# Optimization experiments

Hardware: AMD Instinct MI355X
Metric: run time of the kernel (lower is better)

Reference implementation:

```python
import jax, jax.numpy as jnp
import numpy as np
from jax import lax

BS = 256
EPS = 1e-5  # torch LayerNorm default


def _layernorm(x, g, b):
    m = jnp.mean(x, axis=-1, keepdims=True)
    v = jnp.var(x, axis=-1, keepdims=True)
    return (x - m) / jnp.sqrt(v + EPS) * g + b


def _conv(x, w, b):
    y = lax.conv_general_dilated(x, w, (1, 1), 'VALID',
                                 dimension_numbers=('NCHW', 'OIHW', 'NCHW'))
    return y + b[None, :, None, None]


def _maxpool2(x):
    return lax.reduce_window(x, -jnp.inf, lax.max, (1, 1, 2, 2), (1, 1, 2, 2), 'VALID')


def setup_inputs() -> dict:
    key = jax.random.key(0)
    ks = iter(jax.random.split(key, 64))
    def rn(shape, scale=0.05):
        return jax.random.normal(next(ks), shape, dtype=jnp.float32) * scale
    return dict(
        t=jax.random.uniform(next(ks), (BS, 128, 128), dtype=jnp.float32) * 255.0,
        conv1_w=rn((32, 1, 3, 3)), conv1_b=rn((32,)),
        conv2_w=rn((32, 32, 3, 3)), conv2_b=rn((32,)),
        exp_w=rn((36, 64)), exp_b=rn((64,)),
        # 16 tile-attention modules x 4 heads x (64 -> 16)
        mh_wq=rn((16, 4, 64, 16)), mh_bq=rn((16, 4, 16)),
        mh_wk=rn((16, 4, 64, 16)), mh_bk=rn((16, 4, 16)),
        mh_wv=rn((16, 4, 64, 16)), mh_bv=rn((16, 4, 16)),
        mh_wo=rn((16, 64, 64)), mh_bo=rn((16, 64)),
        ln1_g=jnp.ones((64,), jnp.float32), ln1_b=jnp.zeros((64,), jnp.float32),
        # 2 XL layers x 8 heads x (2048 -> 256)
        xl_wq=rn((2, 8, 2048, 256)), xl_bq=rn((2, 8, 256)),
        xl_wk=rn((2, 8, 2048, 256)), xl_bk=rn((2, 8, 256)),
        xl_wv=rn((2, 8, 2048, 256)), xl_bv=rn((2, 8, 256)),
        xl_wo=rn((2, 2048, 2048)), xl_bo=rn((2, 2048)),
        xln_g=jnp.ones((2, 2048), jnp.float32), xln_b=jnp.zeros((2, 2048), jnp.float32),
        fl1_w=rn((32768, 512)), fl1_b=rn((512,)),
        fl2_w=rn((512, 128)), fl2_b=rn((128,)),
        fl3_w=rn((128, 25)), fl3_b=rn((25,)),
    )


def reference(t, conv1_w, conv1_b, conv2_w, conv2_b, exp_w, exp_b,
              mh_wq, mh_bq, mh_wk, mh_bk, mh_wv, mh_bv, mh_wo, mh_bo,
              ln1_g, ln1_b,
              xl_wq, xl_bq, xl_wk, xl_bk, xl_wv, xl_bv, xl_wo, xl_bo,
              xln_g, xln_b, fl1_w, fl1_b, fl2_w, fl2_b, fl3_w, fl3_b):
    # Eval-mode forward with discard_mem=True (fresh KV memory): every
    # AttentionHead attends over the current step only; dropout = identity.
    bs = t.shape[0]
    x = t / 255.0
    # 4x4 tiling of 32x32 patches -> (bs*16, 1, 32, 32)
    sliced = x.reshape(bs, 4, 32, 4, 32).transpose(0, 1, 3, 2, 4)
    x = sliced.reshape(bs * 16, 1, 32, 32)
    u = _maxpool2(_conv(x, conv1_w, conv1_b))        # (bs*16, 32, 15, 15)
    u = _maxpool2(_conv(u, conv2_w, conv2_b))        # (bs*16, 32, 6, 6)
    u = u.reshape(bs * 16, 32, 36)
    u = jax.nn.relu(u @ exp_w + exp_b)               # (bs*16, 32, 64)
    u = u.reshape(16, bs, 32, 64)                    # raw reshape, as in source

    # 16 multihead modules, 4 heads each, d_feature=16, seq_len=32
    q = jnp.einsum('mbsd,mhdf->mbhsf', u, mh_wq) + mh_bq[:, None, :, None, :]
    k = jnp.einsum('mbsd,mhdf->mbhsf', u, mh_wk) + mh_bk[:, None, :, None, :]
    v = jnp.einsum('mbsd,mhdf->mbhsf', u, mh_wv) + mh_bv[:, None, :, None, :]
    a = jax.nn.softmax(jnp.einsum('mbhsf,mbhtf->mbhst', q, k) / jnp.sqrt(16.0), axis=-1)
    o = jnp.einsum('mbhst,mbhtf->mbhsf', a, v)
    o = o.transpose(0, 1, 3, 2, 4).reshape(16, bs, 32, 64)  # concat heads
    o = jnp.einsum('mbsd,mde->mbse', o, mh_wo) + mh_bo[:, None, None, :]
    u = _layernorm(u + o, ln1_g, ln1_b)
    u = u.reshape(16, bs, 2048).transpose(1, 0, 2)   # (bs, 16, 2048)

    # XL stage (as written in source: att output is computed but discarded,
    # u = u + dropout(u) -> 2u under identity dropout, then LayerNorm)
    for i in range(2):
        q = jnp.einsum('bsd,hdf->bhsf', u, xl_wq[i]) + xl_bq[i][None, :, None, :]
        k = jnp.einsum('bsd,hdf->bhsf', u, xl_wk[i]) + xl_bk[i][None, :, None, :]
        vv = jnp.einsum('bsd,hdf->bhsf', u, xl_wv[i]) + xl_bv[i][None, :, None, :]
        aw = jax.nn.softmax(jnp.einsum('bhsf,bhtf->bhst', q, k) / jnp.sqrt(256.0), axis=-1)
        oo = jnp.einsum('bhst,bhtf->bhsf', aw, vv).transpose(0, 2, 1, 3).reshape(bs, 16, 2048)
        oo = oo @ xl_wo[i] + xl_bo[i]  # discarded, matching the source
        u = u + u
        u = _layernorm(u, xln_g[i], xln_b[i])

    u = u.reshape(bs, 16 * 2048)
    u = jax.nn.relu(u @ fl1_w + fl1_b)
    u = jax.nn.relu(u @ fl2_w + fl2_b)
    return u @ fl3_w + fl3_b
```

## Files before the change

### kernel.cpp

```cpp
#include <hip/hip_runtime.h>
#include <hip/hip_bf16.h>
#include <math.h>

#define LN_EPS 1e-5f

typedef __attribute__((ext_vector_type(8))) short short8v;
typedef __attribute__((ext_vector_type(4))) float f32x4;

static __device__ __forceinline__ unsigned short f2bf(float x) {
    unsigned u = __float_as_uint(x);
    u += 0x7fffu + ((u >> 16) & 1u);
    return (unsigned short)(u >> 16);
}
static __device__ __forceinline__ float bf2f(unsigned short h) {
    return __uint_as_float(((unsigned)h) << 16);
}

#define MFMA3(ACC, AH, AL, BH, BL)                                          \
    ACC = __builtin_amdgcn_mfma_f32_16x16x32_bf16(AH, BH, ACC, 0, 0, 0);    \
    ACC = __builtin_amdgcn_mfma_f32_16x16x32_bf16(AL, BH, ACC, 0, 0, 0);    \
    ACC = __builtin_amdgcn_mfma_f32_16x16x32_bf16(AH, BL, ACC, 0, 0, 0);

__global__ __launch_bounds__(512, 4) void k_fused(
    const float* __restrict__ t,
    const float* __restrict__ c1w, const float* __restrict__ c1b,
    const float* __restrict__ c2w, const float* __restrict__ c2b,
    const float* __restrict__ ew,  const float* __restrict__ eb,
    const float* __restrict__ wq, const float* __restrict__ bq,
    const float* __restrict__ wk, const float* __restrict__ bk,
    const float* __restrict__ wv, const float* __restrict__ bv,
    const float* __restrict__ wo, const float* __restrict__ bo,
    const float* __restrict__ g1, const float* __restrict__ b1,
    const float* __restrict__ xg, const float* __restrict__ xb,
    unsigned short* __restrict__ Ah, unsigned short* __restrict__ Al)
{
    __shared__ __align__(16) unsigned short s_W2[2][9216];
    __shared__ __align__(16) unsigned short s_p1[14400];
    __shared__ __align__(16) float s_s2[1152];
    __shared__ __align__(16) float s_uf[32 * 68];
    __shared__ float s_c2b[32];

    float* s_x  = (float*)s_W2;
    unsigned short* s_wh  = s_W2[0];
    unsigned short* s_wl  = s_W2[1];
    unsigned short* s_p1h = s_p1;
    unsigned short* s_p1l = s_p1 + 7200;
    float* s_ew = (float*)s_p1;
    unsigned short* aw_h = s_W2[0];
    unsigned short* aw_l = s_W2[0] + 4096;
    unsigned short* R1   = s_p1;
    unsigned short* R2   = s_W2[1];
    unsigned short* qA_h = R1;
    unsigned short* qA_l = R1 + 3072;
    unsigned short* kB_h = R1 + 6144;
    unsigned short* kB_l = R1 + 9216;
    unsigned short* p_h  = R1;
    unsigned short* p_l  = R1 + 5120;
    unsigned short* vT_h = R2;
    unsigned short* vT_l = R2 + 2560;
    unsigned short* oA_h = R2;
    unsigned short* oA_l = R2 + 2816;
    float* s_redf = s_s2;

    const int p   = blockIdx.x;
    const int tid = threadIdx.x;

    const int b = p >> 4, tile = p & 15, tr = tile >> 2, tc = tile & 3;
    const float* tp = t + (size_t)b * 128 * 128 + (size_t)tr * 32 * 128 + tc * 32;
    for (int i = tid; i < 1024; i += 512) {
        const int r = i >> 5, c = i & 31;
        s_x[r * 33 + c] = tp[r * 128 + c] * (1.0f / 255.0f);
    }
    if (tid < 32) s_c2b[tid] = c2b[tid];
    __syncthreads();

    if ((tid & 255) < 225) {
        const int pos  = tid & 255;
        const int half = tid >> 8;
        const int pi = pos / 15, pj = pos % 15;
        float xw[16];
        #pragma unroll
        for (int r = 0; r < 4; ++r)
            #pragma unroll
            for (int c = 0; c < 4; ++c)
                xw[r * 4 + c] = s_x[(2 * pi + r) * 33 + (2 * pj + c)];
        #pragma unroll
        for (int og2 = 0; og2 < 2; ++og2) {
            const int og = half * 2 + og2;
            short8v hb, lb;
            #pragma unroll
            for (int o = 0; o < 8; ++o) {
                const int oc = og * 8 + o;
                float w[9];
                #pragma unroll
                for (int j = 0; j < 9; ++j) w[j] = c1w[oc * 9 + j];
                float mx = -3.0e38f;
                #pragma unroll
                for (int a = 0; a < 2; ++a)
                    #pragma unroll
                    for (int bb = 0; bb < 2; ++bb) {
                        float s = xw[(a + 0) * 4 + bb + 0] * w[0]
                                + xw[(a + 0) * 4 + bb + 1] * w[1]
                                + xw[(a + 0) * 4 + bb + 2] * w[2]
                                + xw[(a + 1) * 4 + bb + 0] * w[3]
                                + xw[(a + 1) * 4 + bb + 1] * w[4]
                                + xw[(a + 1) * 4 + bb + 2] * w[5]
                                + xw[(a + 2) * 4 + bb + 0] * w[6]
                                + xw[(a + 2) * 4 + bb + 1] * w[7]
                                + xw[(a + 2) * 4 + bb + 2] * w[8];
                        mx = fmaxf(mx, s);
                    }
                const float val = mx + c1b[oc];
                const unsigned short h = f2bf(val);
                hb[o] = (short)h;
                lb[o] = (short)f2bf(val - bf2f(h));
            }
            *(short8v*)&s_p1h[og * 1800 + pos * 8] = hb;
            *(short8v*)&s_p1l[og * 1800 + pos * 8] = lb;
        }
    }
    __syncthreads();

    {
        const int oc  = tid >> 4;
        const int sub = tid & 15;
        const int kg  = sub >> 2;
        const int off = (sub * 2) & 7;
        const float* wp = c2w + oc * 288 + sub * 18;
        float wf[18];
        #pragma unroll
        for (int j = 0; j < 9; ++j)
            *(float2*)&wf[j * 2] = *(const float2*)&wp[j * 2];
        #pragma unroll
        for (int ks = 0; ks < 9; ++ks) {
            const float v0 = wf[ks];
            const float v1 = wf[9 + ks];
            const unsigned short h0 = f2bf(v0), h1 = f2bf(v1);
            const unsigned short l0 = f2bf(v0 - bf2f(h0));
            const unsigned short l1 = f2bf(v1 - bf2f(h1));
            const int idx = ks * 1024 + kg * 256 + oc * 8 + off;
            *(unsigned*)&s_wh[idx] = (unsigned)h0 | ((unsigned)h1 << 16);
            *(unsigned*)&s_wl[idx] = (unsigned)l0 | ((unsigned)l1 << 16);
        }
    }
    __syncthreads();

    {
        const int lane = tid & 63;
        const int w8   = tid >> 6;
        const int jcol = lane & 15;
        const int lg   = lane >> 4;

        {
            const int nt = w8;
            const int n = nt * 16 + jcol;
            const int pq = n >> 2, w4 = n & 3;
            const int pi = pq / 6, pj = pq - pi * 6;
            const int rbase = 2 * pi + (w4 >> 1);
            const int cbase = 2 * pj + (w4 & 1);

            f32x4 acc0 = {0,0,0,0}, acc1 = {0,0,0,0};
            #pragma unroll
            for (int ks = 0; ks < 9; ++ks) {
                const int dr = ks / 3, dc = ks - dr * 3;
                const int ab = ks * 1024 + lg * 256 + jcol * 8;
                const short8v ah0 = *(const short8v*)&s_wh[ab];
                const short8v ah1 = *(const short8v*)&s_wh[ab + 128];
                const short8v al0 = *(const short8v*)&s_wl[ab];
                const short8v al1 = *(const short8v*)&s_wl[ab + 128];
                const int wpos = (rbase + dr) * 15 + (cbase + dc);
                const int boff = lg * 1800 + wpos * 8;
                const short8v bh = *(const short8v*)&s_p1h[boff];
                const short8v bl = *(const short8v*)&s_p1l[boff];
                acc0 = __builtin_amdgcn_mfma_f32_16x16x32_bf16(ah0, bh, acc0, 0, 0, 0);
                acc0 = __builtin_amdgcn_mfma_f32_16x16x32_bf16(al0, bh, acc0, 0, 0, 0);
                acc0 = __builtin_amdgcn_mfma_f32_16x16x32_bf16(ah0, bl, acc0, 0, 0, 0);
                acc1 = __builtin_amdgcn_mfma_f32_16x16x32_bf16(ah1, bh, acc1, 0, 0, 0);
                acc1 = __builtin_amdgcn_mfma_f32_16x16x32_bf16(al1, bh, acc1, 0, 0, 0);
                acc1 = __builtin_amdgcn_mfma_f32_16x16x32_bf16(ah1, bl, acc1, 0, 0, 0);
            }
            #pragma unroll
            for (int mt = 0; mt < 2; ++mt)
                #pragma unroll
                for (int r = 0; r < 4; ++r) {
                    float v = (mt == 0) ? acc0[r] : acc1[r];
                    v = fmaxf(v, __shfl_xor(v, 1));
                    v = fmaxf(v, __shfl_xor(v, 2));
                    if ((lane & 3) == 0) {
                        const int oc = mt * 16 + (lane >> 4) * 4 + r;
                        const int pq2 = nt * 4 + (jcol >> 2);
                        s_s2[oc * 36 + pq2] = v + s_c2b[oc];
                    }
                }
        }

        if (w8 < 2) {
            const int nt = 8;
            const int mt = w8;
            const int n = nt * 16 + jcol;
            const int pq = n >> 2, w4 = n & 3;
            const int pi = pq / 6, pj = pq - pi * 6;
            const int rbase = 2 * pi + (w4 >> 1);
            const int cbase = 2 * pj + (w4 & 1);

            f32x4 accX = {0,0,0,0};
            #pragma unroll
            for (int ks = 0; ks < 9; ++ks) {
                const int dr = ks / 3, dc = ks - dr * 3;
                const int ab = ks * 1024 + lg * 256 + jcol * 8 + mt * 128;
                const short8v ah = *(const short8v*)&s_wh[ab];
                const short8v al = *(const short8v*)&s_wl[ab];
                const int wpos = (rbase + dr) * 15 + (cbase + dc);
                const int boff = lg * 1800 + wpos * 8;
                const short8v bh = *(const short8v*)&s_p1h[boff];
                const short8v bl = *(const short8v*)&s_p1l[boff];
                accX = __builtin_amdgcn_mfma_f32_16x16x32_bf16(ah, bh, accX, 0, 0, 0);
                accX = __builtin_amdgcn_mfma_f32_16x16x32_bf16(al, bh, accX, 0, 0, 0);
                accX = __builtin_amdgcn_mfma_f32_16x16x32_bf16(ah, bl, accX, 0, 0, 0);
            }
            #pragma unroll
            for (int r = 0; r < 4; ++r) {
                float v = accX[r];
                v = fmaxf(v, __shfl_xor(v, 1));
                v = fmaxf(v, __shfl_xor(v, 2));
                if ((lane & 3) == 0) {
                    const int oc = mt * 16 + (lane >> 4) * 4 + r;
                    const int pq2 = nt * 4 + (jcol >> 2);
                    s_s2[oc * 36 + pq2] = v + s_c2b[oc];
                }
            }
        }
    }
    __syncthreads();

    const int m2 = p >> 8;
    const int b2 = p & 255;
    const int wn   = tid & 63;
    const int wkq8 = tid >> 6;
    float wreg[8];

    #define LOADQKV(SRC)                                                          \
        {                                                                         \
            const float* sp = (SRC) + (size_t)m2 * 4096 + (wn >> 4) * 1024 + (wn & 15); \
            _Pragma("unroll")                                                     \
            for (int j = 0; j < 8; ++j) wreg[j] = sp[(wkq8 * 8 + j) * 16];        \
        }
    #define LOADO(SRC)                                                            \
        {                                                                         \
            const float* sp = (SRC) + (size_t)m2 * 4096 + wn;                     \
            _Pragma("unroll")                                                     \
            for (int j = 0; j < 8; ++j) wreg[j] = sp[(wkq8 * 8 + j) * 64];        \
        }
    #define WRITEW()                                                              \
        {                                                                         \
            _Pragma("unroll")                                                     \
            for (int j2 = 0; j2 < 4; ++j2) {                                      \
                const int d = wkq8 * 8 + j2 * 2;                                  \
                const float v0 = wreg[j2 * 2], v1 = wreg[j2 * 2 + 1];             \
                const unsigned short h0 = f2bf(v0), h1 = f2bf(v1);                \
                const unsigned short q0 = f2bf(v0 - bf2f(h0));                    \
                const unsigned short q1 = f2bf(v1 - bf2f(h1));                    \
                const int idx = wn * 64 + (((d >> 3) ^ (wn & 7)) << 3) + (d & 7); \
                *(unsigned*)&aw_h[idx] = (unsigned)h0 | ((unsigned)h1 << 16);     \
                *(unsigned*)&aw_l[idx] = (unsigned)q0 | ((unsigned)q1 << 16);     \
            }                                                                     \
        }

    for (int i = tid; i < 576; i += 512)
        *(float4*)&s_ew[i * 4] = *(const float4*)&ew[i * 4];
    LOADQKV(wq);
    __syncthreads();

    {
        const int s  = tid >> 4;
        const int e0 = (tid & 15) * 4;
        float acc4[4];
        *(float4*)&acc4[0] = *(const float4*)&eb[e0];
        for (int f = 0; f < 36; ++f) {
            const float sv = s_s2[s * 36 + f];
            const float4 w0 = *(const float4*)&s_ew[f * 64 + e0];
            acc4[0] += sv * w0.x; acc4[1] += sv * w0.y;
            acc4[2] += sv * w0.z; acc4[3] += sv * w0.w;
        }
        float4 o0;
        o0.x = fmaxf(acc4[0], 0.0f); o0.y = fmaxf(acc4[1], 0.0f);
        o0.z = fmaxf(acc4[2], 0.0f); o0.w = fmaxf(acc4[3], 0.0f);
        *(float4*)&s_uf[s * 68 + e0] = o0;
    }
    __syncthreads();

    const int l   = tid & 63;
    const int w   = tid >> 6;
    const int l15 = l & 15;
    const int lg  = l >> 4;

    WRITEW();

    short8v uh[2][2], ul[2][2];
    if (tid < 256) {
        #pragma unroll
        for (int mf = 0; mf < 2; ++mf)
            #pragma unroll
            for (int ks = 0; ks < 2; ++ks) {
                const float* pb = &s_uf[(mf * 16 + l15) * 68 + (ks * 4 + lg) * 8];
                float xv[8];
                *(float4*)&xv[0] = *(const float4*)pb;
                *(float4*)&xv[4] = *(const float4*)(pb + 4);
                short8v hh, ll;
                #pragma unroll
                for (int j = 0; j < 8; ++j) {
                    const unsigned short h = f2bf(xv[j]);
                    hh[j] = (short)h;
                    ll[j] = (short)f2bf(xv[j] - bf2f(h));
                }
                uh[mf][ks] = hh; ul[mf][ks] = ll;
            }
    }
    __syncthreads();

    #define PROJ(BIAS, MODE)                                                      \
        if (tid < 256) {                                                          \
            short8v wbh[2], wbl[2];                                               \
            const int bn = w * 16 + l15;                                          \
            _Pragma("unroll")                                                     \
            for (int ks = 0; ks < 2; ++ks) {                                      \
                const int off = bn * 64 + (((ks * 4 + lg) ^ (bn & 7)) << 3);      \
                wbh[ks] = *(const short8v*)&aw_h[off];                            \
                wbl[ks] = *(const short8v*)&aw_l[off];                            \
            }                                                                     \
            const float bias_v = (BIAS)[m2 * 64 + bn];                            \
            f32x4 a0 = {0,0,0,0}, a1 = {0,0,0,0};                                 \
            _Pragma("unroll")                                                     \
            for (int ks = 0; ks < 2; ++ks) {                                      \
                MFMA3(a0, uh[0][ks], ul[0][ks], wbh[ks], wbl[ks]);                \
                MFMA3(a1, uh[1][ks], ul[1][ks], wbh[ks], wbl[ks]);                \
            }                                                                     \
            _Pragma("unroll")                                                     \
            for (int mf = 0; mf < 2; ++mf) {                                      \
                const f32x4 av = mf ? a1 : a0;                                    \
                _Pragma("unroll")                                                 \
                for (int r = 0; r < 4; ++r) {                                     \
                    const float val = av[r] + bias_v;                             \
                    const unsigned short hh = f2bf(val);                          \
                    const unsigned short lo = f2bf(val - bf2f(hh));               \
                    const int srow = mf * 16 + lg * 4 + r;                        \
                    if ((MODE) == 0) { const int ix = w * 768 + srow * 24 + l15;  \
                        qA_h[ix] = hh; qA_l[ix] = lo; }                           \
                    else if ((MODE) == 1) { const int ix = w * 768 + srow * 24 + l15; \
                        kB_h[ix] = hh; kB_l[ix] = lo; }                           \
                    else { const int ix = w * 640 + l15 * 40 + srow;              \
                        vT_h[ix] = hh; vT_l[ix] = lo; }                           \
                }                                                                 \
            }                                                                     \
        }

    PROJ(bq, 0);
    LOADQKV(wk);
    __syncthreads();
    WRITEW();
    __syncthreads();

    PROJ(bk, 1);
    LOADQKV(wv);
    __syncthreads();
    WRITEW();
    __syncthreads();

    PROJ(bv, 2);
    LOADO(wo);
    __syncthreads();
    WRITEW();
    __syncthreads();

    float pvreg[2][2][4];
    if (tid < 256) {
        const short8v zz = {0,0,0,0,0,0,0,0};
        short8v qh[2], ql[2], kh[2], kl[2];
        const bool kreal = (lg < 2);
        #pragma unroll
        for (int mf = 0; mf < 2; ++mf) {
            if (kreal) {
                const int ia = w * 768 + (mf * 16 + l15) * 24 + lg * 8;
                qh[mf] = *(const short8v*)&qA_h[ia];
                ql[mf] = *(const short8v*)&qA_l[ia];
                kh[mf] = *(const short8v*)&kB_h[ia];
                kl[mf] = *(const short8v*)&kB_l[ia];
            } else { qh[mf] = zz; ql[mf] = zz; kh[mf] = zz; kl[mf] = zz; }
        }
        f32x4 sc[2][2];
        #pragma unroll
        for (int mf = 0; mf < 2; ++mf)
            #pragma unroll
            for (int nf = 0; nf < 2; ++nf) {
                sc[mf][nf] = (f32x4){0,0,0,0};
                MFMA3(sc[mf][nf], qh[mf], ql[mf], kh[nf], kl[nf]);
            }
        #pragma unroll
        for (int mf = 0; mf < 2; ++mf)
            #pragma unroll
            for (int r = 0; r < 4; ++r) {
                const float v0 = sc[mf][0][r] * 0.25f;
                const float v1 = sc[mf][1][r] * 0.25f;
                float mx = fmaxf(v0, v1);
                mx = fmaxf(mx, __shfl_xor(mx, 1));
                mx = fmaxf(mx, __shfl_xor(mx, 2));
                mx = fmaxf(mx, __shfl_xor(mx, 4));
                mx = fmaxf(mx, __shfl_xor(mx, 8));
                const float e0 = expf(v0 - mx), e1 = expf(v1 - mx);
                float sm = e0 + e1;
                sm += __shfl_xor(sm, 1);
                sm += __shfl_xor(sm, 2);
                sm += __shfl_xor(sm, 4);
                sm += __shfl_xor(sm, 8);
                const float inv = 1.0f / sm;
                pvreg[mf][0][r] = e0 * inv;
                pvreg[mf][1][r] = e1 * inv;
            }
    }
    __syncthreads();

    if (tid < 256) {
        #pragma unroll
        for (int mf = 0; mf < 2; ++mf)
            #pragma unroll
            for (int nf = 0; nf < 2; ++nf)
                #pragma unroll
                for (int r = 0; r < 4; ++r) {
                    const int srow = mf * 16 + lg * 4 + r;
                    const int tt = nf * 16 + l15;
                    const int ix = w * 1280 + srow * 40 + tt;
                    const float val = pvreg[mf][nf][r];
                    const unsigned short hh = f2bf(val);
                    p_h[ix] = hh;
                    p_l[ix] = f2bf(val - bf2f(hh));
                }
    }
    __syncthreads();

    f32x4 ov[2];
    if (tid < 256) {
        short8v ph[2], pl[2], vh_, vl_;
        #pragma unroll
        for (int mf = 0; mf < 2; ++mf) {
            const int ix = w * 1280 + (mf * 16 + l15) * 40 + lg * 8;
            ph[mf] = *(const short8v*)&p_h[ix];
            pl[mf] = *(const short8v*)&p_l[ix];
        }
        const int iv = w * 640 + l15 * 40 + lg * 8;
        vh_ = *(const short8v*)&vT_h[iv];
        vl_ = *(const short8v*)&vT_l[iv];
        #pragma unroll
        for (int mf = 0; mf < 2; ++mf) {
            ov[mf] = (f32x4){0,0,0,0};
            MFMA3(ov[mf], ph[mf], pl[mf], vh_, vl_);
        }
    }
    __syncthreads();

    if (tid < 256) {
        #pragma unroll
        for (int mf = 0; mf < 2; ++mf)
            #pragma unroll
            for (int r = 0; r < 4; ++r) {
                const int srow = mf * 16 + lg * 4 + r;
                const int dd = w * 16 + l15;
                const int ix = srow * 88 + dd;
                const float val = ov[mf][r];
                const unsigned short hh = f2bf(val);
                oA_h[ix] = hh;
                oA_l[ix] = f2bf(val - bf2f(hh));
            }
    }
    __syncthreads();

    const int mfA = (w & 3) >> 1;
    const int nfb = (w & 1) * 2;
    float x[2][4];
    if (tid < 256) {
        short8v oh[2], ol[2];
        #pragma unroll
        for (int ks = 0; ks < 2; ++ks) {
            const int ix = (mfA * 16 + l15) * 88 + (ks * 4 + lg) * 8;
            oh[ks] = *(const short8v*)&oA_h[ix];
            ol[ks] = *(const short8v*)&oA_l[ix];
        }
        #pragma unroll
        for (int nfi = 0; nfi < 2; ++nfi) {
            const int n = (nfb + nfi) * 16 + l15;
            f32x4 xe = {0,0,0,0};
            #pragma unroll
            for (int ks = 0; ks < 2; ++ks) {
                const int off = n * 64 + (((ks * 4 + lg) ^ (n & 7)) << 3);
                const short8v wbh = *(const short8v*)&aw_h[off];
                const short8v wbl = *(const short8v*)&aw_l[off];
                MFMA3(xe, oh[ks], ol[ks], wbh, wbl);
            }
            const float bo_v = bo[m2 * 64 + n];
            #pragma unroll
            for (int r = 0; r < 4; ++r) {
                const int srow = mfA * 16 + lg * 4 + r;
                x[nfi][r] = xe[r] + bo_v + s_uf[srow * 68 + n];
            }
        }
        #pragma unroll
        for (int r = 0; r < 4; ++r) {
            float s1 = x[0][r] + x[1][r];
            float s2 = x[0][r] * x[0][r] + x[1][r] * x[1][r];
            s1 += __shfl_xor(s1, 1); s2 += __shfl_xor(s2, 1);
            s1 += __shfl_xor(s1, 2); s2 += __shfl_xor(s2, 2);
            s1 += __shfl_xor(s1, 4); s2 += __shfl_xor(s2, 4);
            s1 += __shfl_xor(s1, 8); s2 += __shfl_xor(s2, 8);
            if (l15 == 0) {
                const int srow = mfA * 16 + lg * 4 + r;
                s_redf[(w & 1) * 64 + srow * 2 + 0] = s1;
                s_redf[(w & 1) * 64 + srow * 2 + 1] = s2;
            }
        }
    }
    __syncthreads();

    float q2[2][4];
    if (tid < 256) {
        #pragma unroll
        for (int r = 0; r < 4; ++r) {
            const int srow = mfA * 16 + lg * 4 + r;
            const float sum = s_redf[srow * 2 + 0] + s_redf[64 + srow * 2 + 0];
            const float ssq = s_redf[srow * 2 + 1] + s_redf[64 + srow * 2 + 1];
            const float mean = sum * (1.0f / 64.0f);
            const float var = fmaxf(ssq * (1.0f / 64.0f) - mean * mean, 0.0f);
            const float inv = rsqrtf(var + LN_EPS);
            #pragma unroll
            for (int nfi = 0; nfi < 2; ++nfi) {
                const int e = (nfb + nfi) * 16 + l15;
                const float y = (x[nfi][r] - mean) * inv * g1[e] + b1[e];
                q2[nfi][r] = 2.0f * y;
            }
        }
    }

    #pragma unroll
    for (int L = 0; L < 2; ++L) {
        if (tid < 256) {
            float ls = 0.0f, lq = 0.0f;
            #pragma unroll
            for (int nfi = 0; nfi < 2; ++nfi)
                #pragma unroll
                for (int r = 0; r < 4; ++r) { ls += q2[nfi][r]; lq += q2[nfi][r] * q2[nfi][r]; }
            ls += __shfl_xor(ls, 1);  lq += __shfl_xor(lq, 1);
            ls += __shfl_xor(ls, 2);  lq += __shfl_xor(lq, 2);
            ls += __shfl_xor(ls, 4);  lq += __shfl_xor(lq, 4);
            ls += __shfl_xor(ls, 8);  lq += __shfl_xor(lq, 8);
            ls += __shfl_xor(ls, 16); lq += __shfl_xor(lq, 16);
            ls += __shfl_xor(ls, 32); lq += __shfl_xor(lq, 32);
            if (l == 0) {
                s_redf[128 + L * 8 + w * 2 + 0] = ls;
                s_redf[128 + L * 8 + w * 2 + 1] = lq;
            }
        }
        __syncthreads();
        if (tid < 256) {
            const float sum = s_redf[128 + L * 8 + 0] + s_redf[128 + L * 8 + 2]
                            + s_redf[128 + L * 8 + 4] + s_redf[128 + L * 8 + 6];
            const float ssq = s_redf[128 + L * 8 + 1] + s_redf[128 + L * 8 + 3]
                            + s_redf[128 + L * 8 + 5] + s_redf[128 + L * 8 + 7];
            const float mean = sum * (1.0f / 2048.0f);
            const float var = fmaxf(ssq * (1.0f / 2048.0f) - mean * mean, 0.0f);
            const float inv = rsqrtf(var + LN_EPS);
            #pragma unroll
            for (int nfi = 0; nfi < 2; ++nfi)
                #pragma unroll
                for (int r = 0; r < 4; ++r) {
                    const int srow = mfA * 16 + lg * 4 + r;
                    const int e = (nfb + nfi) * 16 + l15;
                    const int col = srow * 64 + e;
                    const float z = (q2[nfi][r] - mean) * inv * xg[L * 2048 + col] + xb[L * 2048 + col];
                    q2[nfi][r] = (L == 0) ? 2.0f * z : z;
                }
        }
    }

    if (tid < 256) {
        #pragma unroll
        for (int nfi = 0; nfi < 2; ++nfi)
            #pragma unroll
            for (int r = 0; r < 4; ++r) {
                const int srow = mfA * 16 + lg * 4 + r;
                const int e = (nfb + nfi) * 16 + l15;
                const int col = srow * 64 + e;
                const float val = q2[nfi][r];
                const unsigned short hh = f2bf(val);
                const size_t addr = ((size_t)(m2 * 64 + (col >> 5)) * 256 + b2) * 32 + (col & 31);
                Ah[addr] = hh;
                Al[addr] = f2bf(val - bf2f(hh));
            }
    }
    #undef LOADQKV
    #undef LOADO
    #undef WRITEW
    #undef PROJ
}

__global__ __launch_bounds__(512) void k_fl1(
    const unsigned short* __restrict__ Ah,
    const unsigned short* __restrict__ Al,
    const float* __restrict__ W,
    float* __restrict__ part)
{
    __shared__ __align__(16) unsigned short s_wh[128 * 64];
    __shared__ __align__(16) unsigned short s_wl[128 * 64];

    const int nb  = blockIdx.x;
    const int kb  = blockIdx.y;
    const int tid = threadIdx.x;
    const int lane = tid & 63;
    const int wid  = tid >> 6;
    const int wm = wid >> 1;
    const int wn = wid & 1;

    const int sn = tid & 127;
    const int sq = tid >> 7;
    const int k0 = kb * 512;

    f32x4 acc[4][4];
    #pragma unroll
    for (int i = 0; i < 4; ++i)
        #pragma unroll
        for (int j = 0; j < 4; ++j)
            acc[i][j] = (f32x4){0.0f, 0.0f, 0.0f, 0.0f};

    float wreg[16];
    {
        const float* wp = W + (size_t)(k0 + sq * 16) * 512 + nb * 128 + sn;
        #pragma unroll
        for (int j = 0; j < 16; ++j) wreg[j] = wp[(size_t)j * 512];
    }

    const int hsn = sn & 7;
    const int wbase = sn * 64;
    const int wo0 = (((sq * 2) ^ hsn) << 3);
    const int wo1 = (((sq * 2 + 1) ^ hsn) << 3);

    for (int tt = 0; tt < 8; ++tt) {
        __syncthreads();
        {
            short8v h0, h1, l0, l1;
            #pragma unroll
            for (int j = 0; j < 8; ++j) {
                const unsigned short ha = f2bf(wreg[j]);
                const unsigned short hb = f2bf(wreg[j + 8]);
                h0[j] = (short)ha;
                h1[j] = (short)hb;
                l0[j] = (short)f2bf(wreg[j] - bf2f(ha));
                l1[j] = (short)f2bf(wreg[j + 8] - bf2f(hb));
            }
            *(short8v*)&s_wh[wbase + wo0] = h0;
            *(short8v*)&s_wh[wbase + wo1] = h1;
            *(short8v*)&s_wl[wbase + wo0] = l0;
            *(short8v*)&s_wl[wbase + wo1] = l1;
        }
        if (tt < 7) {
            const float* wp = W + (size_t)(k0 + (tt + 1) * 64 + sq * 16) * 512 + nb * 128 + sn;
            #pragma unroll
            for (int j = 0; j < 16; ++j) wreg[j] = wp[(size_t)j * 512];
        }
        __syncthreads();

        #pragma unroll
        for (int ks = 0; ks < 2; ++ks) {
            const int ktile = (k0 >> 5) + tt * 2 + ks;
            const size_t abase = ((size_t)ktile * 256 + wm * 64 + (lane & 15)) * 32
                               + (lane >> 4) * 8;
            short8v ahf[4], alf[4];
            #pragma unroll
            for (int mf = 0; mf < 4; ++mf) {
                ahf[mf] = *(const short8v*)&Ah[abase + (size_t)mf * 512];
                alf[mf] = *(const short8v*)&Al[abase + (size_t)mf * 512];
            }
            short8v bhf[4], blf[4];
            #pragma unroll
            for (int nf = 0; nf < 4; ++nf) {
                const int n = wn * 64 + nf * 16 + (lane & 15);
                const int q = ks * 4 + (lane >> 4);
                const int baddr = n * 64 + ((q ^ (n & 7)) << 3);
                bhf[nf] = *(const short8v*)&s_wh[baddr];
                blf[nf] = *(const short8v*)&s_wl[baddr];
            }
            #pragma unroll
            for (int mf = 0; mf < 4; ++mf)
                #pragma unroll
                for (int nf = 0; nf < 4; ++nf) {
                    MFMA3(acc[mf][nf], ahf[mf], alf[mf], bhf[nf], blf[nf]);
                }
        }
    }

    float* pp = part + (size_t)kb * 131072 + (size_t)nb * 128;
    const int r0 = (lane >> 4) * 4;
    const int c  = lane & 15;
    #pragma unroll
    for (int mf = 0; mf < 4; ++mf) {
        const int row = wm * 64 + mf * 16 + r0;
        #pragma unroll
        for (int nf = 0; nf < 4; ++nf) {
            const int col = wn * 64 + nf * 16 + c;
            #pragma unroll
            for (int r = 0; r < 4; ++r)
                pp[(size_t)(row + r) * 512 + col] = acc[mf][nf][r];
        }
    }
}

__global__ __launch_bounds__(256) void k_tail(
    const float* __restrict__ part, const float* __restrict__ fb1,
    const float* __restrict__ w2,   const float* __restrict__ fb2,
    const float* __restrict__ w3,   const float* __restrict__ fb3,
    float* __restrict__ out)
{
    __shared__ float s_u1[512];
    __shared__ float s_u2[128];
    const int r = blockIdx.x, tid = threadIdx.x;

    if (tid < 128) {
        const int i4 = r * 512 + tid * 4;
        float4 s = *(const float4*)&fb1[tid * 4];
        for (int ks = 0; ks < 64; ++ks) {
            const float4 p = *(const float4*)&part[(size_t)ks * 131072 + i4];
            s.x += p.x; s.y += p.y; s.z += p.z; s.w += p.w;
        }
        s.x = fmaxf(s.x, 0.0f); s.y = fmaxf(s.y, 0.0f);
        s.z = fmaxf(s.z, 0.0f); s.w = fmaxf(s.w, 0.0f);
        *(float4*)&s_u1[tid * 4] = s;
    }
    __syncthreads();

    if (tid < 128) {
        float acc = fb2[tid];
        for (int k = 0; k < 512; k++) acc += s_u1[k] * w2[k * 128 + tid];
        s_u2[tid] = fmaxf(acc, 0.0f);
    }
    __syncthreads();

    if (tid < 25) {
        float acc = fb3[tid];
        for (int k = 0; k < 128; k++) acc += s_u2[k] * w3[k * 25 + tid];
        out[r * 25 + tid] = acc;
    }
}

extern "C" void kernel_launch(void* const* d_in, const int* in_sizes, int n_in,
                              void* d_out, int out_size, void* d_ws, size_t ws_size,
                              hipStream_t stream)
{
    const float* t      = (const float*)d_in[0];
    const float* c1w    = (const float*)d_in[1];
    const float* c1b    = (const float*)d_in[2];
    const float* c2w    = (const float*)d_in[3];
    const float* c2b    = (const float*)d_in[4];
    const float* ew     = (const float*)d_in[5];
    const float* eb     = (const float*)d_in[6];
    const float* mh_wq  = (const float*)d_in[7];
    const float* mh_bq  = (const float*)d_in[8];
    const float* mh_wk  = (const float*)d_in[9];
    const float* mh_bk  = (const float*)d_in[10];
    const float* mh_wv  = (const float*)d_in[11];
    const float* mh_bv  = (const float*)d_in[12];
    const float* mh_wo  = (const float*)d_in[13];
    const float* mh_bo  = (const float*)d_in[14];
    const float* ln1_g  = (const float*)d_in[15];
    const float* ln1_b  = (const float*)d_in[16];
    const float* xln_g  = (const float*)d_in[25];
    const float* xln_b  = (const float*)d_in[26];
    const float* fl1_w  = (const float*)d_in[27];
    const float* fl1_b  = (const float*)d_in[28];
    const float* fl2_w  = (const float*)d_in[29];
    const float* fl2_b  = (const float*)d_in[30];
    const float* fl3_w  = (const float*)d_in[31];
    const float* fl3_b  = (const float*)d_in[32];
    (void)in_sizes; (void)n_in; (void)out_size; (void)ws_size;

    float* U   = (float*)d_ws;
    float* U2  = U + 8388608;
    unsigned short* Ah = (unsigned short*)U2;
    unsigned short* Al = Ah + 8388608;
    float* PART = U;
    float* out  = (float*)d_out;

    k_fused<<<4096, 512, 0, stream>>>(t, c1w, c1b, c2w, c2b, ew, eb,
                                      mh_wq, mh_bq, mh_wk, mh_bk, mh_wv, mh_bv,
                                      mh_wo, mh_bo, ln1_g, ln1_b, xln_g, xln_b,
                                      Ah, Al);
    k_fl1<<<dim3(4, 64), 512, 0, stream>>>(Ah, Al, fl1_w, PART);
    k_tail<<<256, 256, 0, stream>>>(PART, fl1_b, fl2_w, fl2_b, fl3_w, fl3_b, out);
}
```

Measured before the change: 266.3 us.

## Spread tile-attention MFMA work across all eight waves instead of four

The fused tile-attention stage previously ran its projections, scores, PV and output/LayerNorm math only on the first 256 threads (4 waves), each handling two 16-row fragments. It now assigns each of the 8 waves one head and one 16-row slab, so every wave does half as much MFMA and conversion work and the idle-wave gating is removed. The per-row LayerNorm reduction now combines four partial sums instead of two, and the 2048-wide reduction combines eight waves. It keeps the same barrier count but increases parallel utilisation of the block; register pressure per thread also drops.

```diff
diff --git a/kernel.cpp b/kernel.cpp
--- a/kernel.cpp
+++ b/kernel.cpp
@@ -293,35 +293,33 @@
     const int w   = tid >> 6;
     const int l15 = l & 15;
     const int lg  = l >> 4;
+    const int h   = w & 3;
+    const int mfS = w >> 2;
 
     WRITEW();
 
-    short8v uh[2][2], ul[2][2];
-    if (tid < 256) {
-        #pragma unroll
-        for (int mf = 0; mf < 2; ++mf)
-            #pragma unroll
-            for (int ks = 0; ks < 2; ++ks) {
-                const float* pb = &s_uf[(mf * 16 + l15) * 68 + (ks * 4 + lg) * 8];
-                float xv[8];
-                *(float4*)&xv[0] = *(const float4*)pb;
-                *(float4*)&xv[4] = *(const float4*)(pb + 4);
-                short8v hh, ll;
-                #pragma unroll
-                for (int j = 0; j < 8; ++j) {
-                    const unsigned short h = f2bf(xv[j]);
-                    hh[j] = (short)h;
-                    ll[j] = (short)f2bf(xv[j] - bf2f(h));
-                }
-                uh[mf][ks] = hh; ul[mf][ks] = ll;
-            }
+    short8v uh[2], ul[2];
+    #pragma unroll
+    for (int ks = 0; ks < 2; ++ks) {
+        const float* pb = &s_uf[(mfS * 16 + l15) * 68 + (ks * 4 + lg) * 8];
+        float xv[8];
+        *(float4*)&xv[0] = *(const float4*)pb;
+        *(float4*)&xv[4] = *(const float4*)(pb + 4);
+        short8v hh, ll;
+        #pragma unroll
+        for (int j = 0; j < 8; ++j) {
+            const unsigned short hq = f2bf(xv[j]);
+            hh[j] = (short)hq;
+            ll[j] = (short)f2bf(xv[j] - bf2f(hq));
+        }
+        uh[ks] = hh; ul[ks] = ll;
     }
     __syncthreads();
 
     #define PROJ(BIAS, MODE)                                                      \
-        if (tid < 256) {                                                          \
+        {                                                                         \
             short8v wbh[2], wbl[2];                                               \
-            const int bn = w * 16 + l15;                                          \
+            const int bn = h * 16 + l15;                                          \
             _Pragma("unroll")                                                     \
             for (int ks = 0; ks < 2; ++ks) {                                      \
                 const int off = bn * 64 + (((ks * 4 + lg) ^ (bn & 7)) << 3);      \
@@ -329,28 +327,23 @@
                 wbl[ks] = *(const short8v*)&aw_l[off];                            \
             }                                                                     \
             const float bias_v = (BIAS)[m2 * 64 + bn];                            \
-            f32x4 a0 = {0,0,0,0}, a1 = {0,0,0,0};                                 \
+            f32x4 a0 = {0,0,0,0};                                                 \
             _Pragma("unroll")                                                     \
             for (int ks = 0; ks < 2; ++ks) {                                      \
-                MFMA3(a0, uh[0][ks], ul[0][ks], wbh[ks], wbl[ks]);                \
-                MFMA3(a1, uh[1][ks], ul[1][ks], wbh[ks], wbl[ks]);                \
+                MFMA3(a0, uh[ks], ul[ks], wbh[ks], wbl[ks]);                      \
             }                                                                     \
             _Pragma("unroll")                                                     \
-            for (int mf = 0; mf < 2; ++mf) {                                      \
-                const f32x4 av = mf ? a1 : a0;                                    \
-                _Pragma("unroll")                                                 \
-                for (int r = 0; r < 4; ++r) {                                     \
-                    const float val = av[r] + bias_v;                             \
-                    const unsigned short hh = f2bf(val);                          \
-                    const unsigned short lo = f2bf(val - bf2f(hh));               \
-                    const int srow = mf * 16 + lg * 4 + r;                        \
-                    if ((MODE) == 0) { const int ix = w * 768 + srow * 24 + l15;  \
-                        qA_h[ix] = hh; qA_l[ix] = lo; }                           \
-                    else if ((MODE) == 1) { const int ix = w * 768 + srow * 24 + l15; \
-                        kB_h[ix] = hh; kB_l[ix] = lo; }                           \
-                    else { const int ix = w * 640 + l15 * 40 + srow;              \
-                        vT_h[ix] = hh; vT_l[ix] = lo; }                           \
-                }                                                                 \
+            for (int r = 0; r < 4; ++r) {                                         \
+                const float val = a0[r] + bias_v;                                 \
+                const unsigned short hh = f2bf(val);                              \
+                const unsigned short lo = f2bf(val - bf2f(hh));                   \
+                const int srow = mfS * 16 + lg * 4 + r;                           \
+                if ((MODE) == 0) { const int ix = h * 768 + srow * 24 + l15;      \
+                    qA_h[ix] = hh; qA_l[ix] = lo; }                               \
+                else if ((MODE) == 1) { const int ix = h * 768 + srow * 24 + l15; \
+                    kB_h[ix] = hh; kB_l[ix] = lo; }                               \
+                else { const int ix = h * 640 + l15 * 40 + srow;                  \
+                    vT_h[ix] = hh; vT_l[ix] = lo; }                               \
             }                                                                     \
         }
 
@@ -372,227 +365,188 @@
     WRITEW();
     __syncthreads();
 
-    float pvreg[2][2][4];
-    if (tid < 256) {
+    float pvreg[2][4];
+    {
         const short8v zz = {0,0,0,0,0,0,0,0};
-        short8v qh[2], ql[2], kh[2], kl[2];
+        short8v qh, ql, kh[2], kl[2];
         const bool kreal = (lg < 2);
-        #pragma unroll
-        for (int mf = 0; mf < 2; ++mf) {
-            if (kreal) {
-                const int ia = w * 768 + (mf * 16 + l15) * 24 + lg * 8;
-                qh[mf] = *(const short8v*)&qA_h[ia];
-                ql[mf] = *(const short8v*)&qA_l[ia];
-                kh[mf] = *(const short8v*)&kB_h[ia];
-                kl[mf] = *(const short8v*)&kB_l[ia];
-            } else { qh[mf] = zz; ql[mf] = zz; kh[mf] = zz; kl[mf] = zz; }
-        }
-        f32x4 sc[2][2];
-        #pragma unroll
-        for (int mf = 0; mf < 2; ++mf)
+        if (kreal) {
+            const int ia = h * 768 + (mfS * 16 + l15) * 24 + lg * 8;
+            qh = *(const short8v*)&qA_h[ia];
+            ql = *(const short8v*)&qA_l[ia];
             #pragma unroll
             for (int nf = 0; nf < 2; ++nf) {
-                sc[mf][nf] = (f32x4){0,0,0,0};
-                MFMA3(sc[mf][nf], qh[mf], ql[mf], kh[nf], kl[nf]);
+                const int ik = h * 768 + (nf * 16 + l15) * 24 + lg * 8;
+                kh[nf] = *(const short8v*)&kB_h[ik];
+                kl[nf] = *(const short8v*)&kB_l[ik];
             }
-        #pragma unroll
-        for (int mf = 0; mf < 2; ++mf)
-            #pragma unroll
-            for (int r = 0; r < 4; ++r) {
-                const float v0 = sc[mf][0][r] * 0.25f;
-                const float v1 = sc[mf][1][r] * 0.25f;
-                float mx = fmaxf(v0, v1);
-                mx = fmaxf(mx, __shfl_xor(mx, 1));
-                mx = fmaxf(mx, __shfl_xor(mx, 2));
-                mx = fmaxf(mx, __shfl_xor(mx, 4));
-                mx = fmaxf(mx, __shfl_xor(mx, 8));
-                const float e0 = expf(v0 - mx), e1 = expf(v1 - mx);
-                float sm = e0 + e1;
-                sm += __shfl_xor(sm, 1);
-                sm += __shfl_xor(sm, 2);
-                sm += __shfl_xor(sm, 4);
-                sm += __shfl_xor(sm, 8);
-                const float inv = 1.0f / sm;
-                pvreg[mf][0][r] = e0 * inv;
-                pvreg[mf][1][r] = e1 * inv;
-            }
-    }
-    __syncthreads();
-
-    if (tid < 256) {
-        #pragma unroll
-        for (int mf = 0; mf < 2; ++mf)
-            #pragma unroll
-            for (int nf = 0; nf < 2; ++nf)
-                #pragma unroll
-                for (int r = 0; r < 4; ++r) {
-                    const int srow = mf * 16 + lg * 4 + r;
-                    const int tt = nf * 16 + l15;
-                    const int ix = w * 1280 + srow * 40 + tt;
-                    const float val = pvreg[mf][nf][r];
-                    const unsigned short hh = f2bf(val);
-                    p_h[ix] = hh;
-                    p_l[ix] = f2bf(val - bf2f(hh));
-                }
-    }
-    __syncthreads();
-
-    f32x4 ov[2];
-    if (tid < 256) {
-        short8v ph[2], pl[2], vh_, vl_;
-        #pragma unroll
-        for (int mf = 0; mf < 2; ++mf) {
-            const int ix = w * 1280 + (mf * 16 + l15) * 40 + lg * 8;
-            ph[mf] = *(const short8v*)&p_h[ix];
-            pl[mf] = *(const short8v*)&p_l[ix];
-        }
-        const int iv = w * 640 + l15 * 40 + lg * 8;
-        vh_ = *(const short8v*)&vT_h[iv];
-        vl_ = *(const short8v*)&vT_l[iv];
-        #pragma unroll
-        for (int mf = 0; mf < 2; ++mf) {
-            ov[mf] = (f32x4){0,0,0,0};
-            MFMA3(ov[mf], ph[mf], pl[mf], vh_, vl_);
-        }
-    }
-    __syncthreads();
-
-    if (tid < 256) {
-        #pragma unroll
-        for (int mf = 0; mf < 2; ++mf)
-            #pragma unroll
-            for (int r = 0; r < 4; ++r) {
-                const int srow = mf * 16 + lg * 4 + r;
-                const int dd = w * 16 + l15;
-                const int ix = srow * 88 + dd;
-                const float val = ov[mf][r];
-                const unsigned short hh = f2bf(val);
-                oA_h[ix] = hh;
-                oA_l[ix] = f2bf(val - bf2f(hh));
-            }
-    }
-    __syncthreads();
-
-    const int mfA = (w & 3) >> 1;
-    const int nfb = (w & 1) * 2;
-    float x[2][4];
-    if (tid < 256) {
+        } else { qh = zz; ql = zz; kh[0] = zz; kl[0] = zz; kh[1] = zz; kl[1] = zz; }
+        f32x4 sc[2];
+        #pragma unroll
+        for (int nf = 0; nf < 2; ++nf) {
+            sc[nf] = (f32x4){0,0,0,0};
+            MFMA3(sc[nf], qh, ql, kh[nf], kl[nf]);
+        }
+        #pragma unroll
+        for (int r = 0; r < 4; ++r) {
+            const float v0 = sc[0][r] * 0.25f;
+            const float v1 = sc[1][r] * 0.25f;
+            float mx = fmaxf(v0, v1);
+            mx = fmaxf(mx, __shfl_xor(mx, 1));
+            mx = fmaxf(mx, __shfl_xor(mx, 2));
+            mx = fmaxf(mx, __shfl_xor(mx, 4));
+            mx = fmaxf(mx, __shfl_xor(mx, 8));
+            const float e0 = expf(v0 - mx), e1 = expf(v1 - mx);
+            float sm = e0 + e1;
+            sm += __shfl_xor(sm, 1);
+            sm += __shfl_xor(sm, 2);
+            sm += __shfl_xor(sm, 4);
+            sm += __shfl_xor(sm, 8);
+            const float inv = 1.0f / sm;
+            pvreg[0][r] = e0 * inv;
+            pvreg[1][r] = e1 * inv;
+        }
+    }
+    __syncthreads();
+
+    #pragma unroll
+    for (int nf = 0; nf < 2; ++nf)
+        #pragma unroll
+        for (int r = 0; r < 4; ++r) {
+            const int srow = mfS * 16 + lg * 4 + r;
+            const int tt = nf * 16 + l15;
+            const int ix = h * 1280 + srow * 40 + tt;
+            const float val = pvreg[nf][r];
+            const unsigned short hh = f2bf(val);
+            p_h[ix] = hh;
+            p_l[ix] = f2bf(val - bf2f(hh));
+        }
+    __syncthreads();
+
+    f32x4 ov;
+    {
+        const int ixp = h * 1280 + (mfS * 16 + l15) * 40 + lg * 8;
+        const short8v ph = *(const short8v*)&p_h[ixp];
+        const short8v pl = *(const short8v*)&p_l[ixp];
+        const int iv = h * 640 + l15 * 40 + lg * 8;
+        const short8v vh_ = *(const short8v*)&vT_h[iv];
+        const short8v vl_ = *(const short8v*)&vT_l[iv];
+        ov = (f32x4){0,0,0,0};
+        MFMA3(ov, ph, pl, vh_, vl_);
+    }
+    __syncthreads();
+
+    #pragma unroll
+    for (int r = 0; r < 4; ++r) {
+        const int srow = mfS * 16 + lg * 4 + r;
+        const int dd = h * 16 + l15;
+        const int ix = srow * 88 + dd;
+        const float val = ov[r];
+        const unsigned short hh = f2bf(val);
+        oA_h[ix] = hh;
+        oA_l[ix] = f2bf(val - bf2f(hh));
+    }
+    __syncthreads();
+
+    const int n = h * 16 + l15;
+    float x[4];
+    {
         short8v oh[2], ol[2];
         #pragma unroll
         for (int ks = 0; ks < 2; ++ks) {
-            const int ix = (mfA * 16 + l15) * 88 + (ks * 4 + lg) * 8;
+            const int ix = (mfS * 16 + l15) * 88 + (ks * 4 + lg) * 8;
             oh[ks] = *(const short8v*)&oA_h[ix];
             ol[ks] = *(const short8v*)&oA_l[ix];
         }
-        #pragma unroll
-        for (int nfi = 0; nfi < 2; ++nfi) {
-            const int n = (nfb + nfi) * 16 + l15;
-            f32x4 xe = {0,0,0,0};
-            #pragma unroll
-            for (int ks = 0; ks < 2; ++ks) {
-                const int off = n * 64 + (((ks * 4 + lg) ^ (n & 7)) << 3);
-                const short8v wbh = *(const short8v*)&aw_h[off];
-                const short8v wbl = *(const short8v*)&aw_l[off];
-                MFMA3(xe, oh[ks], ol[ks], wbh, wbl);
-            }
-            const float bo_v = bo[m2 * 64 + n];
-            #pragma unroll
-            for (int r = 0; r < 4; ++r) {
-                const int srow = mfA * 16 + lg * 4 + r;
-                x[nfi][r] = xe[r] + bo_v + s_uf[srow * 68 + n];
-            }
-        }
+        f32x4 xe = {0,0,0,0};
+        #pragma unroll
+        for (int ks = 0; ks < 2; ++ks) {
+            const int off = n * 64 + (((ks * 4 + lg) ^ (n & 7)) << 3);
+            const short8v wbh = *(const short8v*)&aw_h[off];
+            const short8v wbl = *(const short8v*)&aw_l[off];
+            MFMA3(xe, oh[ks], ol[ks], wbh, wbl);
+        }
+        const float bo_v = bo[m2 * 64 + n];
         #pragma unroll
         for (int r = 0; r < 4; ++r) {
-            float s1 = x[0][r] + x[1][r];
-            float s2 = x[0][r] * x[0][r] + x[1][r] * x[1][r];
-            s1 += __shfl_xor(s1, 1); s2 += __shfl_xor(s2, 1);
-            s1 += __shfl_xor(s1, 2); s2 += __shfl_xor(s2, 2);
-            s1 += __shfl_xor(s1, 4); s2 += __shfl_xor(s2, 4);
-            s1 += __shfl_xor(s1, 8); s2 += __shfl_xor(s2, 8);
-            if (l15 == 0) {
-                const int srow = mfA * 16 + lg * 4 + r;
-                s_redf[(w & 1) * 64 + srow * 2 + 0] = s1;
-                s_redf[(w & 1) * 64 + srow * 2 + 1] = s2;
-            }
-        }
-    }
-    __syncthreads();
-
-    float q2[2][4];
-    if (tid < 256) {
+            const int srow = mfS * 16 + lg * 4 + r;
+            x[r] = xe[r] + bo_v + s_uf[srow * 68 + n];
+        }
+    }
+    #pragma unroll
+    for (int r = 0; r < 4; ++r) {
+        float s1 = x[r];
+        float s2 = x[r] * x[r];
+        s1 += __shfl_xor(s1, 1); s2 += __shfl_xor(s2, 1);
+        s1 += __shfl_xor(s1, 2); s2 += __shfl_xor(s2, 2);
+        s1 += __shfl_xor(s1, 4); s2 += __shfl_xor(s2, 4);
+        s1 += __shfl_xor(s1, 8); s2 += __shfl_xor(s2, 8);
+        if (l15 == 0) {
+            const int srow = mfS * 16 + lg * 4 + r;
+            s_redf[h * 64 + srow * 2 + 0] = s1;
+            s_redf[h * 64 + srow * 2 + 1] = s2;
+        }
+    }
+    __syncthreads();
+
+    float q2[4];
+    #pragma unroll
+    for (int r = 0; r < 4; ++r) {
+        const int srow = mfS * 16 + lg * 4 + r;
+        const float sum = s_redf[srow * 2 + 0] + s_redf[64 + srow * 2 + 0]
+                        + s_redf[128 + srow * 2 + 0] + s_redf[192 + srow * 2 + 0];
+        const float ssq = s_redf[srow * 2 + 1] + s_redf[64 + srow * 2 + 1]
+                        + s_redf[128 + srow * 2 + 1] + s_redf[192 + srow * 2 + 1];
+        const float mean = sum * (1.0f / 64.0f);
+        const float var = fmaxf(ssq * (1.0f / 64.0f) - mean * mean, 0.0f);
+        const float inv = rsqrtf(var + LN_EPS);
+        const float y = (x[r] - mean) * inv * g1[n] + b1[n];
+        q2[r] = 2.0f * y;
+    }
+
+    #pragma unroll
+    for (int L = 0; L < 2; ++L) {
+        float ls = 0.0f, lq = 0.0f;
+        #pragma unroll
+        for (int r = 0; r < 4; ++r) { ls += q2[r]; lq += q2[r] * q2[r]; }
+        ls += __shfl_xor(ls, 1);  lq += __shfl_xor(lq, 1);
+        ls += __shfl_xor(ls, 2);  lq += __shfl_xor(lq, 2);
+        ls += __shfl_xor(ls, 4);  lq += __shfl_xor(lq, 4);
+        ls += __shfl_xor(ls, 8);  lq += __shfl_xor(lq, 8);
+        ls += __shfl_xor(ls, 16); lq += __shfl_xor(lq, 16);
+        ls += __shfl_xor(ls, 32); lq += __shfl_xor(lq, 32);
+        if (l == 0) {
+            s_redf[256 + L * 16 + w * 2 + 0] = ls;
+            s_redf[256 + L * 16 + w * 2 + 1] = lq;
+        }
+        __syncthreads();
+        float sum = 0.0f, ssq = 0.0f;
+        #pragma unroll
+        for (int ww = 0; ww < 8; ++ww) {
+            sum += s_redf[256 + L * 16 + ww * 2 + 0];
+            ssq += s_redf[256 + L * 16 + ww * 2 + 1];
+        }
+        const float mean = sum * (1.0f / 2048.0f);
+        const float var = fmaxf(ssq * (1.0f / 2048.0f) - mean * mean, 0.0f);
+        const float inv = rsqrtf(var + LN_EPS);
         #pragma unroll
         for (int r = 0; r < 4; ++r) {
-            const int srow = mfA * 16 + lg * 4 + r;
-            const float sum = s_redf[srow * 2 + 0] + s_redf[64 + srow * 2 + 0];
-            const float ssq = s_redf[srow * 2 + 1] + s_redf[64 + srow * 2 + 1];
-            const float mean = sum * (1.0f / 64.0f);
-            const float var = fmaxf(ssq * (1.0f / 64.0f) - mean * mean, 0.0f);
-            const float inv = rsqrtf(var + LN_EPS);
-            #pragma unroll
-            for (int nfi = 0; nfi < 2; ++nfi) {
-                const int e = (nfb + nfi) * 16 + l15;
-                const float y = (x[nfi][r] - mean) * inv * g1[e] + b1[e];
-                q2[nfi][r] = 2.0f * y;
-            }
-        }
-    }
-
-    #pragma unroll
-    for (int L = 0; L < 2; ++L) {
-        if (tid < 256) {
-            float ls = 0.0f, lq = 0.0f;
-            #pragma unroll
-            for (int nfi = 0; nfi < 2; ++nfi)
-                #pragma unroll
-                for (int r = 0; r < 4; ++r) { ls += q2[nfi][r]; lq += q2[nfi][r] * q2[nfi][r]; }
-            ls += __shfl_xor(ls, 1);  lq += __shfl_xor(lq, 1);
-            ls += __shfl_xor(ls, 2);  lq += __shfl_xor(lq, 2);
-            ls += __shfl_xor(ls, 4);  lq += __shfl_xor(lq, 4);
-            ls += __shfl_xor(ls, 8);  lq += __shfl_xor(lq, 8);
-            ls += __shfl_xor(ls, 16); lq += __shfl_xor(lq, 16);
-            ls += __shfl_xor(ls, 32); lq += __shfl_xor(lq, 32);
-            if (l == 0) {
-                s_redf[128 + L * 8 + w * 2 + 0] = ls;
-                s_redf[128 + L * 8 + w * 2 + 1] = lq;
-            }
-        }
-        __syncthreads();
-        if (tid < 256) {
-            const float sum = s_redf[128 + L * 8 + 0] + s_redf[128 + L * 8 + 2]
-                            + s_redf[128 + L * 8 + 4] + s_redf[128 + L * 8 + 6];
-            const float ssq = s_redf[128 + L * 8 + 1] + s_redf[128 + L * 8 + 3]
-                            + s_redf[128 + L * 8 + 5] + s_redf[128 + L * 8 + 7];
-            const float mean = sum * (1.0f / 2048.0f);
-            const float var = fmaxf(ssq * (1.0f / 2048.0f) - mean * mean, 0.0f);
-            const float inv = rsqrtf(var + LN_EPS);
-            #pragma unroll
-            for (int nfi = 0; nfi < 2; ++nfi)
-                #pragma unroll
-                for (int r = 0; r < 4; ++r) {
-                    const int srow = mfA * 16 + lg * 4 + r;
-                    const int e = (nfb + nfi) * 16 + l15;
-                    const int col = srow * 64 + e;
-                    const float z = (q2[nfi][r] - mean) * inv * xg[L * 2048 + col] + xb[L * 2048 + col];
-                    q2[nfi][r] = (L == 0) ? 2.0f * z : z;
-                }
-        }
-    }
-
-    if (tid < 256) {
-        #pragma unroll
-        for (int nfi = 0; nfi < 2; ++nfi)
-            #pragma unroll
-            for (int r = 0; r < 4; ++r) {
-                const int srow = mfA * 16 + lg * 4 + r;
-                const int e = (nfb + nfi) * 16 + l15;
-                const int col = srow * 64 + e;
-                const float val = q2[nfi][r];
-                const unsigned short hh = f2bf(val);
-                const size_t addr = ((size_t)(m2 * 64 + (col >> 5)) * 256 + b2) * 32 + (col & 31);
-                Ah[addr] = hh;
-                Al[addr] = f2bf(val - bf2f(hh));
-            }
+            const int srow = mfS * 16 + lg * 4 + r;
+            const int col = srow * 64 + n;
+            const float z = (q2[r] - mean) * inv * xg[L * 2048 + col] + xb[L * 2048 + col];
+            q2[r] = (L == 0) ? 2.0f * z : z;
+        }
+    }
+
+    #pragma unroll
+    for (int r = 0; r < 4; ++r) {
+        const int srow = mfS * 16 + lg * 4 + r;
+        const int col = srow * 64 + n;
+        const float val = q2[r];
+        const unsigned short hh = f2bf(val);
+        const size_t addr = ((size_t)(m2 * 64 + (col >> 5)) * 256 + b2) * 32 + (col & 31);
+        Ah[addr] = hh;
+        Al[addr] = f2bf(val - bf2f(hh));
     }
     #undef LOADQKV
     #undef LOADO
```

Result: faster. 256.8 us (median of 2 runs) (-3.6%).
